# Performance work log

Hardware: AMD Instinct MI355X
Metric: run time of the kernel (lower is better)

The kernel has to match this reference:

```python
import jax, jax.numpy as jnp
import numpy as np

BASE_WEIGHT = 0.01
ADAPTATION_RATE = 0.1
EPS = 1e-8
N = 16384
H = 64


def setup_inputs() -> dict:
    key = jax.random.key(0)
    k1, k2, k3, k4 = jax.random.split(key, 4)
    return {
        "x_input": jax.random.normal(k1, (N,), dtype=jnp.float32),
        "targets": jax.random.normal(k2, (N,), dtype=jnp.float32),
        "w1": jax.random.normal(k3, (H,), dtype=jnp.float32) * 0.5,
        "b1": jnp.zeros((H,), dtype=jnp.float32),
        "w2": jax.random.normal(k4, (H,), dtype=jnp.float32) * 0.5,
        "b2": jnp.zeros((1,), dtype=jnp.float32),
    }


def _mlp(x, w1, b1, w2, b2):
    # elementwise 1 -> H -> 1 tanh MLP: predictions y_i = f(x_i)
    h = jnp.tanh(x[:, None] * w1 + b1)  # [N, H]
    return h @ w2 + b2[0]               # [N]


def _local_density(x):
    # NxN pairwise abs-diff matrix, top-3 smallest per row
    diff = jnp.abs(x[:, None] - x[None, :]) + EPS       # [N, N]
    neg_knn, _ = jax.lax.top_k(-diff, 3)                # smallest 3 via negation
    knn = -neg_knn                                       # [N, 3]
    dens = 1.0 / (knn.mean(axis=1, keepdims=True) + EPS)  # [N, 1]
    return dens / (dens.max() + EPS)


def reference(x_input, targets, w1, b1, w2, b2):
    f_sum = lambda xx: jnp.sum(_mlp(xx, w1, b1, w2, b2))
    predictions = _mlp(x_input, w1, b1, w2, b2)
    mse_loss = jnp.mean((predictions - targets) ** 2)

    # torch.autograd.grad(..., grad_outputs=ones) twice == grad of summed output twice
    dy_dx_sum = lambda xx: jnp.sum(jax.grad(f_sum)(xx))
    d2y_dx2 = jax.grad(dy_dx_sum)(x_input)               # [N]

    density = _local_density(x_input)                    # [N, 1]
    adaptive_weights = 1.0 + ADAPTATION_RATE * density   # [N, 1]
    # torch broadcasts [N,1]*[N] -> [N,N]; mean of that outer product equals
    # mean(weights) * mean(d2**2) exactly, so compute it without the NxN alloc.
    curvature_penalty = BASE_WEIGHT * (jnp.mean(adaptive_weights) * jnp.mean(d2y_dx2 ** 2))

    total_loss = mse_loss + curvature_penalty
    return (total_loss, mse_loss, curvature_penalty)
```

## Files before the change

kernel.cpp:

```cpp
#include <hip/hip_runtime.h>
#include <math.h>

#define NPTS 16384
#define HDIM 64
#define JCH 16
#define CHUNK (NPTS / JCH)
#define IBLK 256
#define EPSF 1e-8f
#define FMAX3 3.402823466e38f

__device__ __forceinline__ void ins3(float& m1, float& m2, float& m3, float d) {
    m3 = __builtin_amdgcn_fmed3f(d, m2, m3);
    m2 = __builtin_amdgcn_fmed3f(d, m1, m2);
    m1 = fminf(d, m1);
}

__global__ __launch_bounds__(IBLK) void knn_partial_kernel(
    const float* __restrict__ x, float* __restrict__ part, float* __restrict__ acc) {
    const int jc = blockIdx.x & (JCH - 1);
    const int ic = blockIdx.x >> 4;
    if (blockIdx.x == 0 && threadIdx.x < 8) acc[threadIdx.x] = 0.0f;

    const int i = ic * IBLK + threadIdx.x;
    const float xi = x[i];
    const float* __restrict__ xc = x + jc * CHUNK;
    float a1 = FMAX3, a2 = FMAX3, a3 = FMAX3;
    float c1 = FMAX3, c2 = FMAX3, c3 = FMAX3;
#pragma unroll 8
    for (int k = 0; k < CHUNK; k += 2) {
        float d0 = fabsf(xi - xc[k]);
        float d1 = fabsf(xi - xc[k + 1]);
        ins3(a1, a2, a3, d0);
        ins3(c1, c2, c3, d1);
    }
    ins3(a1, a2, a3, c1);
    ins3(a1, a2, a3, c2);
    ins3(a1, a2, a3, c3);
    part[(jc * 3 + 0) * NPTS + i] = a1;
    part[(jc * 3 + 1) * NPTS + i] = a2;
    part[(jc * 3 + 2) * NPTS + i] = a3;
}

__global__ __launch_bounds__(64) void fuse_kernel(
    const float* __restrict__ x, const float* __restrict__ tg,
    const float* __restrict__ w1, const float* __restrict__ b1,
    const float* __restrict__ w2, const float* __restrict__ b2,
    const float* __restrict__ part, float* __restrict__ acc,
    float* __restrict__ out) {
    __shared__ float sw1[HDIM], sb1[HDIM], sw2[HDIM], sc[HDIM];
    const int t = threadIdx.x;
    sw1[t] = w1[t];
    sb1[t] = b1[t];
    sw2[t] = w2[t];
    sc[t] = w2[t] * w1[t] * w1[t];
    __syncthreads();

    const int i = blockIdx.x * 64 + t;

    float m1 = FMAX3, m2 = FMAX3, m3 = FMAX3;
#pragma unroll
    for (int jc = 0; jc < JCH; ++jc) {
        float p1 = part[(jc * 3 + 0) * NPTS + i];
        float p2 = part[(jc * 3 + 1) * NPTS + i];
        float p3 = part[(jc * 3 + 2) * NPTS + i];
        ins3(m1, m2, m3, p1);
        ins3(m1, m2, m3, p2);
        ins3(m1, m2, m3, p3);
    }
    float sum3 = m1 + m2 + m3;
    float dens = 1.0f / (sum3 * (1.0f / 3.0f) + 2.0f * EPSF);

    const float xi = x[i];
    float y = b2[0];
    float d2a = 0.0f;
#pragma unroll 8
    for (int j = 0; j < HDIM; ++j) {
        float u = fmaf(xi, sw1[j], sb1[j]);
        float e = __expf(2.0f * u);
        float r = __builtin_amdgcn_rcpf(e + 1.0f);
        float tt = fmaf(-2.0f, r, 1.0f);
        y = fmaf(sw2[j], tt, y);
        float s = tt * tt;
        float g = 2.0f * tt * (s - 1.0f);
        d2a = fmaf(sc[j], g, d2a);
    }
    float diff = y - tg[i];
    float msep = diff * diff;
    float d2sq = d2a * d2a;

    float rs_mse = msep, rs_d2 = d2sq, rs_dn = dens, rmx = dens;
    for (int o = 32; o > 0; o >>= 1) {
        rs_mse += __shfl_down(rs_mse, o);
        rs_d2 += __shfl_down(rs_d2, o);
        rs_dn += __shfl_down(rs_dn, o);
        rmx = fmaxf(rmx, __shfl_down(rmx, o));
    }
    if (t == 0) {
        atomicAdd(&acc[0], rs_mse);
        atomicAdd(&acc[1], rs_d2);
        atomicAdd(&acc[2], rs_dn);
        atomicMax((unsigned int*)&acc[3], __float_as_uint(rmx));
        __threadfence();
        unsigned int ticket = atomicAdd((unsigned int*)&acc[4], 1u);
        if (ticket == gridDim.x - 1) {
            float s_mse = atomicAdd(&acc[0], 0.0f);
            float s_d2 = atomicAdd(&acc[1], 0.0f);
            float s_dn = atomicAdd(&acc[2], 0.0f);
            float dmax = __uint_as_float(atomicMax((unsigned int*)&acc[3], 0u));
            float mse = s_mse * (1.0f / NPTS);
            float md2 = s_d2 * (1.0f / NPTS);
            float mean_density = (s_dn * (1.0f / NPTS)) / (dmax + EPSF);
            float mean_w = 1.0f + 0.1f * mean_density;
            float penalty = 0.01f * mean_w * md2;
            out[0] = mse + penalty;
            out[1] = mse;
            out[2] = penalty;
        }
    }
}

extern "C" void kernel_launch(void* const* d_in, const int* in_sizes, int n_in,
                              void* d_out, int out_size, void* d_ws, size_t ws_size,
                              hipStream_t stream) {
    const float* x = (const float*)d_in[0];
    const float* tg = (const float*)d_in[1];
    const float* w1 = (const float*)d_in[2];
    const float* b1 = (const float*)d_in[3];
    const float* w2 = (const float*)d_in[4];
    const float* b2 = (const float*)d_in[5];
    float* out = (float*)d_out;
    float* wsf = (float*)d_ws;
    float* part = wsf;
    float* acc = wsf + JCH * 3 * NPTS;

    hipLaunchKernelGGL(knn_partial_kernel, dim3((NPTS / IBLK) * JCH), dim3(IBLK), 0, stream,
                       x, part, acc);
    hipLaunchKernelGGL(fuse_kernel, dim3(NPTS / 64), dim3(64), 0, stream,
                       x, tg, w1, b1, w2, b2, part, acc, out);
}
```

Before: 111.8 us.

## Fuse kNN and MLP into one kernel and track only the two nearest neighbours

```diff
diff --git a/kernel.cpp b/kernel.cpp
--- a/kernel.cpp
+++ b/kernel.cpp
@@ -3,118 +3,107 @@
 
 #define NPTS 16384
 #define HDIM 64
-#define JCH 16
-#define CHUNK (NPTS / JCH)
-#define IBLK 256
+#define NSEG 8
+#define SEGLEN (NPTS / NSEG)
+#define IBLK 512
+#define NBLK (NPTS / 64)
 #define EPSF 1e-8f
 #define FMAX3 3.402823466e38f
 
-__device__ __forceinline__ void ins3(float& m1, float& m2, float& m3, float d) {
-    m3 = __builtin_amdgcn_fmed3f(d, m2, m3);
+__device__ __forceinline__ void ins2(float& m1, float& m2, float d) {
     m2 = __builtin_amdgcn_fmed3f(d, m1, m2);
     m1 = fminf(d, m1);
 }
 
-__global__ __launch_bounds__(IBLK) void knn_partial_kernel(
-    const float* __restrict__ x, float* __restrict__ part, float* __restrict__ acc) {
-    const int jc = blockIdx.x & (JCH - 1);
-    const int ic = blockIdx.x >> 4;
-    if (blockIdx.x == 0 && threadIdx.x < 8) acc[threadIdx.x] = 0.0f;
-
-    const int i = ic * IBLK + threadIdx.x;
-    const float xi = x[i];
-    const float* __restrict__ xc = x + jc * CHUNK;
-    float a1 = FMAX3, a2 = FMAX3, a3 = FMAX3;
-    float c1 = FMAX3, c2 = FMAX3, c3 = FMAX3;
-#pragma unroll 8
-    for (int k = 0; k < CHUNK; k += 2) {
-        float d0 = fabsf(xi - xc[k]);
-        float d1 = fabsf(xi - xc[k + 1]);
-        ins3(a1, a2, a3, d0);
-        ins3(c1, c2, c3, d1);
-    }
-    ins3(a1, a2, a3, c1);
-    ins3(a1, a2, a3, c2);
-    ins3(a1, a2, a3, c3);
-    part[(jc * 3 + 0) * NPTS + i] = a1;
-    part[(jc * 3 + 1) * NPTS + i] = a2;
-    part[(jc * 3 + 2) * NPTS + i] = a3;
-}
-
-__global__ __launch_bounds__(64) void fuse_kernel(
+__global__ __launch_bounds__(IBLK) void fused_kernel(
     const float* __restrict__ x, const float* __restrict__ tg,
     const float* __restrict__ w1, const float* __restrict__ b1,
     const float* __restrict__ w2, const float* __restrict__ b2,
-    const float* __restrict__ part, float* __restrict__ acc,
-    float* __restrict__ out) {
-    __shared__ float sw1[HDIM], sb1[HDIM], sw2[HDIM], sc[HDIM];
+    float* __restrict__ acc, float* __restrict__ out) {
+    __shared__ float sA[NSEG][64], sB[NSEG][64];
     const int t = threadIdx.x;
-    sw1[t] = w1[t];
-    sb1[t] = b1[t];
-    sw2[t] = w2[t];
-    sc[t] = w2[t] * w1[t] * w1[t];
+    const int lane = t & 63;
+    const int w = t >> 6;
+    const int ib = blockIdx.x;
+    const int i = ib * 64 + lane;
+    const float xi = x[i];
+    const float* __restrict__ xc = x + w * SEGLEN;
+
+    float m1 = FMAX3, m2 = FMAX3;
+    if (w == (ib >> 5)) {
+        float m3 = FMAX3;
+#pragma unroll 16
+        for (int k = 0; k < SEGLEN; ++k) {
+            float d = fabsf(xi - xc[k]);
+            m3 = __builtin_amdgcn_fmed3f(d, m2, m3);
+            m2 = __builtin_amdgcn_fmed3f(d, m1, m2);
+            m1 = fminf(d, m1);
+        }
+        m1 = m2;
+        m2 = m3;
+    } else {
+#pragma unroll 16
+        for (int k = 0; k < SEGLEN; ++k) {
+            float d = fabsf(xi - xc[k]);
+            ins2(m1, m2, d);
+        }
+    }
+    sA[w][lane] = m1;
+    sB[w][lane] = m2;
     __syncthreads();
 
-    const int i = blockIdx.x * 64 + t;
+    if (t < 64) {
+        float M1 = FMAX3, M2 = FMAX3;
+#pragma unroll
+        for (int s = 0; s < NSEG; ++s) {
+            ins2(M1, M2, sA[s][t]);
+            ins2(M1, M2, sB[s][t]);
+        }
+        float dens = 1.0f / ((M1 + M2) * (1.0f / 3.0f) + 2.0f * EPSF);
 
-    float m1 = FMAX3, m2 = FMAX3, m3 = FMAX3;
-#pragma unroll
-    for (int jc = 0; jc < JCH; ++jc) {
-        float p1 = part[(jc * 3 + 0) * NPTS + i];
-        float p2 = part[(jc * 3 + 1) * NPTS + i];
-        float p3 = part[(jc * 3 + 2) * NPTS + i];
-        ins3(m1, m2, m3, p1);
-        ins3(m1, m2, m3, p2);
-        ins3(m1, m2, m3, p3);
-    }
-    float sum3 = m1 + m2 + m3;
-    float dens = 1.0f / (sum3 * (1.0f / 3.0f) + 2.0f * EPSF);
-
-    const float xi = x[i];
-    float y = b2[0];
-    float d2a = 0.0f;
+        float y = b2[0];
+        float d2a = 0.0f;
 #pragma unroll 8
-    for (int j = 0; j < HDIM; ++j) {
-        float u = fmaf(xi, sw1[j], sb1[j]);
-        float e = __expf(2.0f * u);
-        float r = __builtin_amdgcn_rcpf(e + 1.0f);
-        float tt = fmaf(-2.0f, r, 1.0f);
-        y = fmaf(sw2[j], tt, y);
-        float s = tt * tt;
-        float g = 2.0f * tt * (s - 1.0f);
-        d2a = fmaf(sc[j], g, d2a);
-    }
-    float diff = y - tg[i];
-    float msep = diff * diff;
-    float d2sq = d2a * d2a;
-
-    float rs_mse = msep, rs_d2 = d2sq, rs_dn = dens, rmx = dens;
-    for (int o = 32; o > 0; o >>= 1) {
-        rs_mse += __shfl_down(rs_mse, o);
-        rs_d2 += __shfl_down(rs_d2, o);
-        rs_dn += __shfl_down(rs_dn, o);
-        rmx = fmaxf(rmx, __shfl_down(rmx, o));
-    }
-    if (t == 0) {
-        atomicAdd(&acc[0], rs_mse);
-        atomicAdd(&acc[1], rs_d2);
-        atomicAdd(&acc[2], rs_dn);
-        atomicMax((unsigned int*)&acc[3], __float_as_uint(rmx));
-        __threadfence();
-        unsigned int ticket = atomicAdd((unsigned int*)&acc[4], 1u);
-        if (ticket == gridDim.x - 1) {
-            float s_mse = atomicAdd(&acc[0], 0.0f);
-            float s_d2 = atomicAdd(&acc[1], 0.0f);
-            float s_dn = atomicAdd(&acc[2], 0.0f);
-            float dmax = __uint_as_float(atomicMax((unsigned int*)&acc[3], 0u));
-            float mse = s_mse * (1.0f / NPTS);
-            float md2 = s_d2 * (1.0f / NPTS);
-            float mean_density = (s_dn * (1.0f / NPTS)) / (dmax + EPSF);
-            float mean_w = 1.0f + 0.1f * mean_density;
-            float penalty = 0.01f * mean_w * md2;
-            out[0] = mse + penalty;
-            out[1] = mse;
-            out[2] = penalty;
+        for (int j = 0; j < HDIM; ++j) {
+            float a1 = w1[j], bb = b1[j], a2 = w2[j];
+            float u = fmaf(xi, a1, bb);
+            float e = __expf(2.0f * u);
+            float r = __builtin_amdgcn_rcpf(e + 1.0f);
+            float tt = fmaf(-2.0f, r, 1.0f);
+            y = fmaf(a2, tt, y);
+            float g = 2.0f * tt * fmaf(tt, tt, -1.0f);
+            d2a = fmaf(a2 * a1 * a1, g, d2a);
+        }
+        float diff = y - tg[i];
+        float rs_mse = diff * diff;
+        float rs_d2 = d2a * d2a;
+        float rs_dn = dens, rmx = dens;
+        for (int o = 32; o > 0; o >>= 1) {
+            rs_mse += __shfl_down(rs_mse, o);
+            rs_d2 += __shfl_down(rs_d2, o);
+            rs_dn += __shfl_down(rs_dn, o);
+            rmx = fmaxf(rmx, __shfl_down(rmx, o));
+        }
+        if (t == 0) {
+            atomicAdd(&acc[0], rs_mse);
+            atomicAdd(&acc[1], rs_d2);
+            atomicAdd(&acc[2], rs_dn);
+            atomicMax((unsigned int*)&acc[3], __float_as_uint(rmx));
+            __threadfence();
+            unsigned int ticket = atomicAdd((unsigned int*)&acc[4], 1u);
+            if (ticket == NBLK - 1) {
+                float s_mse = atomicAdd(&acc[0], 0.0f);
+                float s_d2 = atomicAdd(&acc[1], 0.0f);
+                float s_dn = atomicAdd(&acc[2], 0.0f);
+                float dmax = __uint_as_float(atomicMax((unsigned int*)&acc[3], 0u));
+                float mse = s_mse * (1.0f / NPTS);
+                float md2 = s_d2 * (1.0f / NPTS);
+                float mean_density = (s_dn * (1.0f / NPTS)) / (dmax + EPSF);
+                float penalty = 0.01f * (1.0f + 0.1f * mean_density) * md2;
+                out[0] = mse + penalty;
+                out[1] = mse;
+                out[2] = penalty;
+            }
         }
     }
 }
@@ -129,12 +118,9 @@
     const float* w2 = (const float*)d_in[4];
     const float* b2 = (const float*)d_in[5];
     float* out = (float*)d_out;
-    float* wsf = (float*)d_ws;
-    float* part = wsf;
-    float* acc = wsf + JCH * 3 * NPTS;
+    float* acc = (float*)d_ws;
 
-    hipLaunchKernelGGL(knn_partial_kernel, dim3((NPTS / IBLK) * JCH), dim3(IBLK), 0, stream,
-                       x, part, acc);
-    hipLaunchKernelGGL(fuse_kernel, dim3(NPTS / 64), dim3(64), 0, stream,
-                       x, tg, w1, b1, w2, b2, part, acc, out);
+    hipMemsetAsync(acc, 0, 8 * sizeof(float), stream);
+    hipLaunchKernelGGL(fused_kernel, dim3(NBLK), dim3(IBLK), 0, stream,
+                       x, tg, w1, b1, w2, b2, acc, out);
 }
```

New measurement: 120.6 us. +7.9%, slower.
